# Kernel tuning notes

Hardware: AMD Instinct MI355X
Metric: run time of the kernel (lower is better)

Reference implementation:

```python
import jax, jax.numpy as jnp
import numpy as np

S = 3072        # packed sequence length
DIM = 1280      # hidden size
H = 16          # num heads
HD = DIM // H   # head dim = 80
NSEG = 3        # number of packed segments


def setup_inputs() -> dict:
    key = jax.random.key(0)
    ks = jax.random.split(key, 6)
    hidden_states = jax.random.normal(ks[0], (S, DIM), jnp.float32)
    cos = jax.random.uniform(ks[1], (S, HD), jnp.float32, minval=-1.0, maxval=1.0)
    sin = jax.random.uniform(ks[2], (S, HD), jnp.float32, minval=-1.0, maxval=1.0)
    qkv_w = jax.random.normal(ks[3], (3 * DIM, DIM), jnp.float32) * 0.02
    qkv_b = jnp.zeros((3 * DIM,), jnp.float32)
    proj_w = jax.random.normal(ks[4], (DIM, DIM), jnp.float32) * 0.02
    proj_b = jnp.zeros((DIM,), jnp.float32)
    # 3 equal segments; cu_seqlens = [0, 1024, 2048, 3072]
    cu_seqlens = jnp.arange(NSEG + 1, dtype=jnp.int32) * (S // NSEG)
    return {
        "hidden_states": hidden_states, "cos": cos, "sin": sin,
        "qkv_w": qkv_w, "qkv_b": qkv_b, "proj_w": proj_w, "proj_b": proj_b,
        "cu_seqlens": cu_seqlens,
    }


def rotate_half(x):
    x1, x2 = jnp.split(x, 2, axis=-1)
    return jnp.concatenate((-x2, x1), axis=-1)


def reference(hidden_states, cos, sin, qkv_w, qkv_b, proj_w, proj_b, cu_seqlens):
    seq = hidden_states.shape[0]
    # QKV projection: [S, 3*DIM] -> [S, 3, H, HD]
    qkv = (hidden_states @ qkv_w.T + qkv_b).reshape(seq, 3, H, HD)
    q, k, v = qkv[:, 0], qkv[:, 1], qkv[:, 2]  # each [S, H, HD]
    # RoPE in float32, cos/sin broadcast over heads via [S, 1, HD]
    c = cos[:, None, :].astype(jnp.float32)
    s = sin[:, None, :].astype(jnp.float32)
    qf, kf = q.astype(jnp.float32), k.astype(jnp.float32)
    q = (qf * c + rotate_half(qf) * s).astype(q.dtype)
    k = (kf * c + rotate_half(kf) * s).astype(k.dtype)
    # Block-diagonal additive mask from cu_seqlens (vectorized, no loop)
    pos = jnp.arange(seq)
    seg = jnp.searchsorted(cu_seqlens, pos, side="right")  # segment id per token
    neg = jnp.finfo(jnp.float32).min
    mask = jnp.where(seg[:, None] == seg[None, :], 0.0, neg)  # [S, S]
    # Dense attention over packed sequence
    scores = jnp.einsum("shd,thd->hst", q, k) / np.sqrt(HD).astype(np.float32)
    scores = scores + mask  # broadcast over heads
    attn = jax.nn.softmax(scores.astype(jnp.float32), axis=-1).astype(q.dtype)
    out = jnp.einsum("hst,thd->shd", attn, v).reshape(seq, DIM)
    return out @ proj_w.T + proj_b
```

## Files before the change

kernel.cpp:

```cpp
#include <hip/hip_runtime.h>
#include <hip/hip_bf16.h>


#define S_TOT 3072
#define DIM   1280
#define NH    16
#define HD    80
#define SEG   1024
#define TDIM  3840

typedef short v8s __attribute__((ext_vector_type(8)));
typedef float v4f __attribute__((ext_vector_type(4)));

__device__ __forceinline__ short f2bf(float v) {
  __hip_bfloat16 b = __float2bfloat16(v);
  return *reinterpret_cast<short*>(&b);
}

__device__ __forceinline__ float bf2f(short s) {
  unsigned u = ((unsigned)(unsigned short)s) << 16;
  float f;
  __builtin_memcpy(&f, &u, 4);
  return f;
}

__device__ __forceinline__ void gload16(const void* g, void* lds) {
  __builtin_amdgcn_global_load_lds(
      (const __attribute__((address_space(1))) char*)g,
      (__attribute__((address_space(3))) char*)lds, 16, 0, 0);
}

#define CVT_N1 (S_TOT * DIM / 4)
#define CVT_N2 (TDIM * DIM / 4)
#define CVT_N3 (DIM * DIM / 4)
__global__ __launch_bounds__(256) void cvt3(const float* __restrict__ in1,
                                            const float* __restrict__ in2,
                                            const float* __restrict__ in3,
                                            __hip_bfloat16* __restrict__ o1,
                                            __hip_bfloat16* __restrict__ o2,
                                            __hip_bfloat16* __restrict__ o3) {
  int i = blockIdx.x * 256 + threadIdx.x;
  const float* in;
  __hip_bfloat16* out;
  if (i < CVT_N1) { in = in1; out = o1; }
  else if (i < CVT_N1 + CVT_N2) { in = in2; out = o2; i -= CVT_N1; }
  else { in = in3; out = o3; i -= CVT_N1 + CVT_N2; }
  const float4 v = ((const float4*)in)[i];
  __hip_bfloat162 p0, p1;
  p0.x = __float2bfloat16(v.x); p0.y = __float2bfloat16(v.y);
  p1.x = __float2bfloat16(v.z); p1.y = __float2bfloat16(v.w);
  __hip_bfloat162* o = (__hip_bfloat162*)(out + (size_t)i * 4);
  o[0] = p0; o[1] = p1;
}

extern __shared__ short ring[];

__global__ __launch_bounds__(512, 2) void gemm1_p(const __hip_bfloat16* __restrict__ A,
                                                  const __hip_bfloat16* __restrict__ B,
                                                  const float* __restrict__ bias,
                                                  __hip_bfloat16* __restrict__ C,
                                                  int M, int N, int K) {
  const int tid  = threadIdx.x;
  const int wave = tid >> 6;
  const int lane = tid & 63;
  const int quad = lane >> 4;
  const int l16  = lane & 15;
  const int wmp  = wave >> 2;
  const int wnp  = wave & 3;

  {
  }
  const int l   = blockIdx.x;
  const int xcd = l & 7;
  const int sq  = l >> 3;
  const int rb  = xcd & 3;
  const int cb  = xcd >> 2;
  int bxi, byi;
  if (cb == 0)       { bxi = 3 * rb + sq % 3; byi = sq / 3; }
  else if (sq < 21)  { bxi = 3 * rb + sq % 3; byi = 8 + sq / 3; }
  else               { bxi = 3 * rb + 2;      byi = 7; }
  const int bm = bxi * 256;
  const int bn = byi * 256;

  const int srow = tid >> 2;
  const int sc   = tid & 3;
  const int kc   = sc ^ (srow & 3) ^ ((srow >> 2) & 3);
  const short* aA0 = (const short*)A + (size_t)(bm + srow) * K + kc * 8;
  const short* aA1 = aA0 + (size_t)128 * K;
  const short* bB0 = (const short*)B + (size_t)(bn + srow) * K + kc * 8;
  const short* bB1 = bB0 + (size_t)128 * K;
  const int wst = wave * 512;

#define STAGE1(t) do {                                   \
    short* rb_ = ring + (((t) & 3) * 16384);             \
    const int ko_ = (t) * 32;                            \
    gload16(aA0 + ko_, rb_ + wst);                       \
    gload16(aA1 + ko_, rb_ + 4096 + wst);                \
    gload16(bB0 + ko_, rb_ + 8192 + wst);                \
    gload16(bB1 + ko_, rb_ + 12288 + wst);               \
  } while (0)

  v4f acc[8][4];
  const v4f vz = {0.f, 0.f, 0.f, 0.f};
  #pragma unroll
  for (int i = 0; i < 8; ++i)
    #pragma unroll
    for (int j = 0; j < 4; ++j) acc[i][j] = vz;

  const int nt  = K >> 5;
  const int khx = quad ^ (l16 & 3) ^ ((l16 >> 2) & 3);

  STAGE1(0); STAGE1(1); STAGE1(2);

  for (int t = 0; t < nt; ++t) {
    const int rem = nt - 1 - t;
    if (rem >= 2)      asm volatile("s_waitcnt vmcnt(8)" ::: "memory");
    else if (rem == 1) asm volatile("s_waitcnt vmcnt(4)" ::: "memory");
    else               asm volatile("s_waitcnt vmcnt(0)" ::: "memory");
    __builtin_amdgcn_s_barrier();
    __builtin_amdgcn_sched_barrier(0);

    const short* rb2 = ring + ((t & 3) * 16384);
    v8s afr[8], bfr[4];
    #pragma unroll
    for (int i = 0; i < 8; ++i)
      afr[i] = *(const v8s*)&rb2[((wmp * 128 + i * 16 + l16) * 4 + khx) * 8];
    #pragma unroll
    for (int j = 0; j < 4; ++j)
      bfr[j] = *(const v8s*)&rb2[8192 + ((wnp * 64 + j * 16 + l16) * 4 + khx) * 8];
    __builtin_amdgcn_s_setprio(1);
    #pragma unroll
    for (int i = 0; i < 8; ++i)
      #pragma unroll
      for (int j = 0; j < 4; ++j)
        acc[i][j] = __builtin_amdgcn_mfma_f32_16x16x32_bf16(afr[i], bfr[j], acc[i][j], 0, 0, 0);
    __builtin_amdgcn_s_setprio(0);

    __builtin_amdgcn_sched_barrier(0);
    __builtin_amdgcn_s_barrier();
    __builtin_amdgcn_sched_barrier(0);
    if (t + 3 < nt) STAGE1(t + 3);
  }
#undef STAGE1

  #pragma unroll
  for (int j = 0; j < 4; ++j) {
    const int col = bn + wnp * 64 + j * 16 + l16;
    const float bj = bias[col];
    #pragma unroll
    for (int i = 0; i < 8; ++i) {
      const int row0 = bm + wmp * 128 + i * 16 + quad * 4;
      #pragma unroll
      for (int r = 0; r < 4; ++r)
        C[(size_t)(row0 + r) * N + col] = __float2bfloat16(acc[i][j][r] + bj);
    }
  }
}

__global__ __launch_bounds__(256) void gemm2_c(const __hip_bfloat16* __restrict__ A,
                                               const __hip_bfloat16* __restrict__ B,
                                               const float* __restrict__ bias,
                                               float* __restrict__ C,
                                               int M, int N, int K) {
  __shared__ __align__(16) short Abuf[2][4096];
  __shared__ __align__(16) short Bbuf[2][8192];
  const int tid  = threadIdx.x;
  const int wave = tid >> 6;
  const int lane = tid & 63;
  const int quad = lane >> 4;
  const int l16  = lane & 15;
  const int bm = blockIdx.x * 64;
  const int bn = blockIdx.y * 128;
  const int wm = (wave & 1) * 32;
  const int wn = (wave >> 1) * 64;

  const int srow = tid >> 3;
  const int skh  = tid & 7;
  const __hip_bfloat16* Ag[2];
  const __hip_bfloat16* Bg[4];
  int Ao[2], Bo[4];
  #pragma unroll
  for (int l = 0; l < 2; ++l) {
    const int row = l * 32 + srow;
    Ag[l] = A + (size_t)(bm + row) * K + skh * 8;
    Ao[l] = (row * 8 + (skh ^ (row & 7))) * 8;
  }
  #pragma unroll
  for (int l = 0; l < 4; ++l) {
    const int row = l * 32 + srow;
    Bg[l] = B + (size_t)(bn + row) * K + skh * 8;
    Bo[l] = (row * 8 + (skh ^ (row & 7))) * 8;
  }

  v4f acc[2][4];
  const v4f vz = {0.f, 0.f, 0.f, 0.f};
  #pragma unroll
  for (int i = 0; i < 2; ++i)
    #pragma unroll
    for (int j = 0; j < 4; ++j) acc[i][j] = vz;

  const int sw = l16 & 7;
  const int nk = K >> 6;
  v8s ra[2], rb[4];

  #pragma unroll
  for (int l = 0; l < 2; ++l) ra[l] = *(const v8s*)Ag[l];
  #pragma unroll
  for (int l = 0; l < 4; ++l) rb[l] = *(const v8s*)Bg[l];
  #pragma unroll
  for (int l = 0; l < 2; ++l) *(v8s*)&Abuf[0][Ao[l]] = ra[l];
  #pragma unroll
  for (int l = 0; l < 4; ++l) *(v8s*)&Bbuf[0][Bo[l]] = rb[l];
  __syncthreads();

  for (int k = 0; k < nk; ++k) {
    const int cur = k & 1;
    const bool more = (k + 1 < nk);
    if (more) {
      const int off = (k + 1) * 64;
      #pragma unroll
      for (int l = 0; l < 2; ++l) ra[l] = *(const v8s*)(Ag[l] + off);
      #pragma unroll
      for (int l = 0; l < 4; ++l) rb[l] = *(const v8s*)(Bg[l] + off);
    }
    #pragma unroll
    for (int s = 0; s < 2; ++s) {
      const int khx = (s * 4 + quad) ^ sw;
      v8s af[2], bf[4];
      #pragma unroll
      for (int i = 0; i < 2; ++i)
        af[i] = *(const v8s*)&Abuf[cur][((wm + i * 16 + l16) * 8 + khx) * 8];
      #pragma unroll
      for (int j = 0; j < 4; ++j)
        bf[j] = *(const v8s*)&Bbuf[cur][((wn + j * 16 + l16) * 8 + khx) * 8];
      #pragma unroll
      for (int i = 0; i < 2; ++i)
        #pragma unroll
        for (int j = 0; j < 4; ++j)
          acc[i][j] = __builtin_amdgcn_mfma_f32_16x16x32_bf16(af[i], bf[j], acc[i][j], 0, 0, 0);
    }
    if (more) {
      #pragma unroll
      for (int l = 0; l < 2; ++l) *(v8s*)&Abuf[1 - cur][Ao[l]] = ra[l];
      #pragma unroll
      for (int l = 0; l < 4; ++l) *(v8s*)&Bbuf[1 - cur][Bo[l]] = rb[l];
    }
    __syncthreads();
  }

  #pragma unroll
  for (int j = 0; j < 4; ++j) {
    const int col = bn + wn + j * 16 + l16;
    const float bj = bias[col];
    #pragma unroll
    for (int i = 0; i < 2; ++i) {
      const int row0 = bm + wm + i * 16 + quad * 4;
      #pragma unroll
      for (int r = 0; r < 4; ++r)
        C[(size_t)(row0 + r) * N + col] = acc[i][j][r] + bj;
    }
  }
}

#define QK_BLOCKS ((2 * S_TOT * 16 * 12) / 256)
#define V_BLOCKS  ((3 * 16 * 16 * 8 * 96) / 256)
__global__ __launch_bounds__(256) void pack_all(const __hip_bfloat16* __restrict__ qkv,
                                                const float* __restrict__ cos_,
                                                const float* __restrict__ sin_,
                                                short* __restrict__ Qp,
                                                short* __restrict__ Kp,
                                                short* __restrict__ Vp) {
  const int bid = blockIdx.x;
  if (bid < QK_BLOCKS) {
    const int idx = bid * 256 + threadIdx.x;
    const int kd = idx % 12;
    const int h  = (idx / 12) % 16;
    const int s  = (idx / 192) % S_TOT;
    const int p  = idx / (192 * S_TOT);
    const int seg = s >> 10, tb = (s >> 6) & 15, t = s & 63;
    short* out = (p ? Kp : Qp) +
                 ((size_t)(((seg * 16 + h) * 16 + tb) * 12 + kd) * 64 + t) * 8;
    short tmp[8];
    if (kd >= 10) {
      #pragma unroll
      for (int j = 0; j < 8; ++j) tmp[j] = 0;
      *(int4*)out = *(int4*)tmp;
      return;
    }
    const short* row = (const short*)qkv + (size_t)s * TDIM + p * DIM + h * HD;
    const int d0 = kd * 8;
    const v8s xm = *(const v8s*)(row + d0);
    const v8s xr = *(const v8s*)(row + d0 + ((kd < 5) ? 40 : -40));
    const float sgn = (kd < 5) ? -1.f : 1.f;
    const float scale = (p == 0) ? 0.111803398874989485f : 1.0f;
    #pragma unroll
    for (int j = 0; j < 8; ++j) {
      const int d = d0 + j;
      const float v = (bf2f(xm[j]) * cos_[s * HD + d] +
                       sgn * bf2f(xr[j]) * sin_[s * HD + d]) * scale;
      tmp[j] = f2bf(v);
    }
    *(int4*)out = *(int4*)tmp;
  } else {
    const int idx = (bid - QK_BLOCKS) * 256 + threadIdx.x;
    const int d  = idx % 96;
    const int td = (idx / 96) % 8;
    const int tb = (idx / 768) % 16;
    const int h  = (idx / (768 * 16)) % 16;
    const int seg = idx / (768 * 256);
    const int s0 = seg * SEG + tb * 64 + td * 8;
    const short* q = (const short*)qkv;
    short tmp[8];
    if (d < 80) {
      #pragma unroll
      for (int j = 0; j < 8; ++j)
        tmp[j] = q[(size_t)(s0 + j) * TDIM + 2 * DIM + h * HD + d];
    } else {
      const short fill = (d == 80) ? (short)0x3F80 : (short)0;
      #pragma unroll
      for (int j = 0; j < 8; ++j) tmp[j] = fill;
    }
    *(int4*)(Vp + (size_t)idx * 8) = *(int4*)tmp;
  }
}

__global__ __launch_bounds__(256, 4) void attn_mfma(const short* __restrict__ Qp,
                                                    const short* __restrict__ Kp,
                                                    const short* __restrict__ Vp,
                                                    __hip_bfloat16* __restrict__ out) {
  __shared__ __align__(16) short Ks[64 * 96];
  __shared__ __align__(16) short Vs[64 * 96];
  __shared__ __align__(16) short Ps[4][16 * 68];

  const int l   = blockIdx.x;
  const int xcd = l & 7;
  const int j8  = l >> 3;
  const int g   = xcd * 6 + (j8 >> 4);
  const int qt  = j8 & 15;
  const int h   = g & 15;
  const int seg = g >> 4;
  const int tid  = threadIdx.x;
  const int wave = tid >> 6;
  const int lane = tid & 63;
  const int quad = lane >> 4;
  const int l16  = lane & 15;
  const int sh16 = g;

  const short* Qg = Qp + (size_t)(sh16 * 16 + qt) * 6144;
  const short* Kg = Kp + (size_t)sh16 * 16 * 6144;
  const short* Vg = Vp + (size_t)sh16 * 16 * 6144;

  v8s af[3];
  #pragma unroll
  for (int ks = 0; ks < 3; ++ks)
    af[ks] = *(const v8s*)(Qg + ((ks * 4 + quad) * 64 + wave * 16 + l16) * 8);

  v8s kr[3], vr[3];
  #pragma unroll
  for (int it = 0; it < 3; ++it) {
    const int o = (it * 256 + tid) * 8;
    kr[it] = *(const v8s*)(Kg + o);
    vr[it] = *(const v8s*)(Vg + o);
  }
  #pragma unroll
  for (int it = 0; it < 3; ++it) {
    const int o = (it * 256 + tid) * 8;
    *(v8s*)&Ks[o] = kr[it];
    *(v8s*)&Vs[o] = vr[it];
  }
  __syncthreads();

  v4f o4[6];
  const v4f vz = {0.f, 0.f, 0.f, 0.f};
  #pragma unroll
  for (int n = 0; n < 6; ++n) o4[n] = vz;

  for (int kb = 0; kb < 16; ++kb) {
    const bool more = (kb + 1 < 16);
    if (more) {
      const size_t base = (size_t)(kb + 1) * 6144;
      #pragma unroll
      for (int it = 0; it < 3; ++it) {
        const int o = (it * 256 + tid) * 8;
        kr[it] = *(const v8s*)(Kg + base + o);
        vr[it] = *(const v8s*)(Vg + base + o);
      }
    }

    v4f s4[4];
    #pragma unroll
    for (int j = 0; j < 4; ++j) {
      s4[j] = vz;
      #pragma unroll
      for (int ks = 0; ks < 3; ++ks) {
        const v8s bf = *(const v8s*)&Ks[((ks * 4 + quad) * 64 + j * 16 + l16) * 8];
        s4[j] = __builtin_amdgcn_mfma_f32_16x16x32_bf16(af[ks], bf, s4[j], 0, 0, 0);
      }
    }

    #pragma unroll
    for (int reg = 0; reg < 4; ++reg)
      #pragma unroll
      for (int j = 0; j < 4; ++j)
        Ps[wave][(quad * 4 + reg) * 68 + j * 16 + l16] = f2bf(__expf(s4[j][reg]));

    v8s pa[2];
    #pragma unroll
    for (int kp = 0; kp < 2; ++kp)
      pa[kp] = *(const v8s*)&Ps[wave][l16 * 68 + kp * 32 + quad * 8];
    #pragma unroll
    for (int n = 0; n < 6; ++n) {
      #pragma unroll
      for (int kp = 0; kp < 2; ++kp) {
        const v8s vb = *(const v8s*)&Vs[((kp * 4 + quad) * 96 + n * 16 + l16) * 8];
        o4[n] = __builtin_amdgcn_mfma_f32_16x16x32_bf16(pa[kp], vb, o4[n], 0, 0, 0);
      }
    }

    __syncthreads();
    if (more) {
      #pragma unroll
      for (int it = 0; it < 3; ++it) {
        const int o = (it * 256 + tid) * 8;
        *(v8s*)&Ks[o] = kr[it];
        *(v8s*)&Vs[o] = vr[it];
      }
    }
    __syncthreads();
  }

  float inv[4];
  #pragma unroll
  for (int r = 0; r < 4; ++r)
    inv[r] = 1.f / __shfl(o4[5][r], quad << 4);
  const int row0 = seg * SEG + qt * 64 + wave * 16 + quad * 4;
  #pragma unroll
  for (int n = 0; n < 5; ++n) {
    const int col = h * HD + n * 16 + l16;
    #pragma unroll
    for (int r = 0; r < 4; ++r)
      out[(size_t)(row0 + r) * DIM + col] = __float2bfloat16(o4[n][r] * inv[r]);
  }
}

extern "C" void kernel_launch(void* const* d_in, const int* in_sizes, int n_in,
                              void* d_out, int out_size, void* d_ws, size_t ws_size,
                              hipStream_t stream) {
  (void)in_sizes; (void)n_in; (void)out_size; (void)ws_size;
  const float* hs     = (const float*)d_in[0];
  const float* cosp   = (const float*)d_in[1];
  const float* sinp   = (const float*)d_in[2];
  const float* qkv_w  = (const float*)d_in[3];
  const float* qkv_b  = (const float*)d_in[4];
  const float* proj_w = (const float*)d_in[5];
  const float* proj_b = (const float*)d_in[6];

  float* out_f = (float*)d_out;
  __hip_bfloat16* qkv_b16 = (__hip_bfloat16*)d_ws;
  __hip_bfloat16* hs_b    = qkv_b16 + (size_t)S_TOT * TDIM;
  __hip_bfloat16* qkvw_b  = hs_b + (size_t)S_TOT * DIM;
  __hip_bfloat16* projw_b = qkvw_b + (size_t)TDIM * DIM;
  short* Qp = (short*)qkvw_b;
  short* Kp = (short*)(projw_b + (size_t)DIM * DIM);
  short* Vp = Kp + (size_t)3 * 16 * 16 * 6144;
  __hip_bfloat16* attn_b = hs_b;

  static bool attr_set = false;
  if (!attr_set) {
    hipFuncSetAttribute((const void*)gemm1_p,
                        hipFuncAttributeMaxDynamicSharedMemorySize, 131072);
    attr_set = true;
  }

  cvt3<<<(CVT_N1 + CVT_N2 + CVT_N3) / 256, 256, 0, stream>>>(
      hs, qkv_w, proj_w, hs_b, qkvw_b, projw_b);

  gemm1_p<<<dim3(180), 512, 131072, stream>>>(
      hs_b, qkvw_b, qkv_b, qkv_b16, S_TOT, TDIM, DIM);

  pack_all<<<QK_BLOCKS + V_BLOCKS, 256, 0, stream>>>(qkv_b16, cosp, sinp, Qp, Kp, Vp);

  attn_mfma<<<dim3(768), 256, 0, stream>>>(Qp, Kp, Vp, attn_b);

  gemm2_c<<<dim3(S_TOT / 64, DIM / 128), 256, 0, stream>>>(
      attn_b, projw_b, proj_b, out_f, S_TOT, DIM, DIM);
}
```

Baseline: 213.7 us.

## Restructure QKV GEMM to 3-stage ring with single barrier and new swizzle

Replaces the 4-buffer LDS ring with a 3-buffer ring that issues the next prefetch before the MFMA work and uses one barrier per iteration instead of two. It also changes the LDS swizzle and row mapping, hardcodes K, and drops the XCD-aware block remap in favour of a plain 2D grid. Cutting dynamic LDS from 128KB to 96KB may improve occupancy and reduce synchronization. The risks are bank conflicts from the new layout and worse L2 locality without the XCD remap.

Result: faster. 204.3 us (-4.4%).

```diff
diff --git a/kernel.cpp b/kernel.cpp
--- a/kernel.cpp
+++ b/kernel.cpp
@@ -8,6 +8,7 @@
 #define HD    80
 #define SEG   1024
 #define TDIM  3840
+#define K1    1280
 
 typedef short v8s __attribute__((ext_vector_type(8)));
 typedef float v4f __attribute__((ext_vector_type(4)));
@@ -55,11 +56,10 @@
 
 extern __shared__ short ring[];
 
-__global__ __launch_bounds__(512, 2) void gemm1_p(const __hip_bfloat16* __restrict__ A,
-                                                  const __hip_bfloat16* __restrict__ B,
-                                                  const float* __restrict__ bias,
-                                                  __hip_bfloat16* __restrict__ C,
-                                                  int M, int N, int K) {
+__global__ __launch_bounds__(512, 2) void gemm1_3r(const __hip_bfloat16* __restrict__ A,
+                                                   const __hip_bfloat16* __restrict__ B,
+                                                   const float* __restrict__ bias,
+                                                   __hip_bfloat16* __restrict__ C) {
   const int tid  = threadIdx.x;
   const int wave = tid >> 6;
   const int lane = tid & 63;
@@ -67,38 +67,29 @@
   const int l16  = lane & 15;
   const int wmp  = wave >> 2;
   const int wnp  = wave & 3;
-
-  {
-  }
-  const int l   = blockIdx.x;
-  const int xcd = l & 7;
-  const int sq  = l >> 3;
-  const int rb  = xcd & 3;
-  const int cb  = xcd >> 2;
-  int bxi, byi;
-  if (cb == 0)       { bxi = 3 * rb + sq % 3; byi = sq / 3; }
-  else if (sq < 21)  { bxi = 3 * rb + sq % 3; byi = 8 + sq / 3; }
-  else               { bxi = 3 * rb + 2;      byi = 7; }
-  const int bm = bxi * 256;
-  const int bn = byi * 256;
-
-  const int srow = tid >> 2;
-  const int sc   = tid & 3;
-  const int kc   = sc ^ (srow & 3) ^ ((srow >> 2) & 3);
-  const short* aA0 = (const short*)A + (size_t)(bm + srow) * K + kc * 8;
-  const short* aA1 = aA0 + (size_t)128 * K;
-  const short* bB0 = (const short*)B + (size_t)(bn + srow) * K + kc * 8;
-  const short* bB1 = bB0 + (size_t)128 * K;
+  const int bm = blockIdx.x * 256;
+  const int bn = blockIdx.y * 256;
+
+  const int r0 = ((tid >> 3) << 1) + ((tid >> 2) & 1);
+  const int gs = (tid & 3) ^ ((tid >> 3) & 3);
+  const short* A0 = (const short*)A + (size_t)(bm + r0) * K1 + gs * 8;
+  const short* A1 = A0 + (size_t)128 * K1;
+  const short* B0 = (const short*)B + (size_t)(bn + r0) * K1 + gs * 8;
+  const short* B1 = B0 + (size_t)128 * K1;
   const int wst = wave * 512;
 
-#define STAGE1(t) do {                                   \
-    short* rb_ = ring + (((t) & 3) * 16384);             \
-    const int ko_ = (t) * 32;                            \
-    gload16(aA0 + ko_, rb_ + wst);                       \
-    gload16(aA1 + ko_, rb_ + 4096 + wst);                \
-    gload16(bB0 + ko_, rb_ + 8192 + wst);                \
-    gload16(bB1 + ko_, rb_ + 12288 + wst);               \
+#define STG(sbuf, ko) do {                              \
+    short* d_ = ring + (sbuf) * 16384;                  \
+    gload16(A0 + (ko), d_ + wst);                       \
+    gload16(A1 + (ko), d_ + 4096 + wst);                \
+    gload16(B0 + (ko), d_ + 8192 + wst);                \
+    gload16(B1 + (ko), d_ + 12288 + wst);               \
   } while (0)
+
+  const int posA  = quad ^ ((l16 >> 1) & 3);
+  const int rbase = (l16 >> 1) * 64 + (l16 & 1) * 32 + posA * 8;
+  const int Abase = wmp * 4096 + rbase;
+  const int Bbase = 8192 + wnp * 2048 + rbase;
 
   v4f acc[8][4];
   const v4f vz = {0.f, 0.f, 0.f, 0.f};
@@ -107,41 +98,41 @@
     #pragma unroll
     for (int j = 0; j < 4; ++j) acc[i][j] = vz;
 
-  const int nt  = K >> 5;
-  const int khx = quad ^ (l16 & 3) ^ ((l16 >> 2) & 3);
-
-  STAGE1(0); STAGE1(1); STAGE1(2);
-
-  for (int t = 0; t < nt; ++t) {
-    const int rem = nt - 1 - t;
-    if (rem >= 2)      asm volatile("s_waitcnt vmcnt(8)" ::: "memory");
-    else if (rem == 1) asm volatile("s_waitcnt vmcnt(4)" ::: "memory");
-    else               asm volatile("s_waitcnt vmcnt(0)" ::: "memory");
-    __builtin_amdgcn_s_barrier();
-    __builtin_amdgcn_sched_barrier(0);
-
-    const short* rb2 = ring + ((t & 3) * 16384);
-    v8s afr[8], bfr[4];
+  STG(0, 0);
+  STG(1, 32);
+  asm volatile("s_waitcnt vmcnt(4)" ::: "memory");
+  __builtin_amdgcn_s_barrier();
+  __builtin_amdgcn_sched_barrier(0);
+
+  int cb = 0, sb = 2;
+  for (int t = 0; t < 40; ++t) {
+    if (t + 2 < 40) STG(sb, (t + 2) * 32);
+
+    const short* lb = ring + cb * 16384;
+    v8s af[8], bf[4];
+    #pragma unroll
+    for (int i = 0; i < 8; ++i) af[i] = *(const v8s*)&lb[Abase + i * 512];
+    #pragma unroll
+    for (int j = 0; j < 4; ++j) bf[j] = *(const v8s*)&lb[Bbase + j * 512];
+
+    __builtin_amdgcn_s_setprio(1);
     #pragma unroll
     for (int i = 0; i < 8; ++i)
-      afr[i] = *(const v8s*)&rb2[((wmp * 128 + i * 16 + l16) * 4 + khx) * 8];
-    #pragma unroll
-    for (int j = 0; j < 4; ++j)
-      bfr[j] = *(const v8s*)&rb2[8192 + ((wnp * 64 + j * 16 + l16) * 4 + khx) * 8];
-    __builtin_amdgcn_s_setprio(1);
-    #pragma unroll
-    for (int i = 0; i < 8; ++i)
       #pragma unroll
       for (int j = 0; j < 4; ++j)
-        acc[i][j] = __builtin_amdgcn_mfma_f32_16x16x32_bf16(afr[i], bfr[j], acc[i][j], 0, 0, 0);
+        acc[i][j] = __builtin_amdgcn_mfma_f32_16x16x32_bf16(af[i], bf[j], acc[i][j], 0, 0, 0);
     __builtin_amdgcn_s_setprio(0);
 
-    __builtin_amdgcn_sched_barrier(0);
-    __builtin_amdgcn_s_barrier();
-    __builtin_amdgcn_sched_barrier(0);
-    if (t + 3 < nt) STAGE1(t + 3);
-  }
-#undef STAGE1
+    if (t < 39) {
+      if (t + 2 < 40) asm volatile("s_waitcnt vmcnt(4)" ::: "memory");
+      else            asm volatile("s_waitcnt vmcnt(0)" ::: "memory");
+      __builtin_amdgcn_s_barrier();
+      __builtin_amdgcn_sched_barrier(0);
+    }
+    cb = (cb == 2) ? 0 : cb + 1;
+    sb = (sb == 2) ? 0 : sb + 1;
+  }
+#undef STG
 
   #pragma unroll
   for (int j = 0; j < 4; ++j) {
@@ -152,7 +143,7 @@
       const int row0 = bm + wmp * 128 + i * 16 + quad * 4;
       #pragma unroll
       for (int r = 0; r < 4; ++r)
-        C[(size_t)(row0 + r) * N + col] = __float2bfloat16(acc[i][j][r] + bj);
+        C[(size_t)(row0 + r) * TDIM + col] = __float2bfloat16(acc[i][j][r] + bj);
     }
   }
 }
@@ -467,16 +458,16 @@
 
   static bool attr_set = false;
   if (!attr_set) {
-    hipFuncSetAttribute((const void*)gemm1_p,
-                        hipFuncAttributeMaxDynamicSharedMemorySize, 131072);
+    hipFuncSetAttribute((const void*)gemm1_3r,
+                        hipFuncAttributeMaxDynamicSharedMemorySize, 98304);
     attr_set = true;
   }
 
   cvt3<<<(CVT_N1 + CVT_N2 + CVT_N3) / 256, 256, 0, stream>>>(
       hs, qkv_w, proj_w, hs_b, qkvw_b, projw_b);
 
-  gemm1_p<<<dim3(180), 512, 131072, stream>>>(
-      hs_b, qkvw_b, qkv_b, qkv_b16, S_TOT, TDIM, DIM);
+  gemm1_3r<<<dim3(S_TOT / 256, TDIM / 256), 512, 98304, stream>>>(
+      hs_b, qkvw_b, qkv_b, qkv_b16);
 
   pack_all<<<QK_BLOCKS + V_BLOCKS, 256, 0, stream>>>(qkv_b16, cosp, sinp, Qp, Kp, Vp);
 
```
